# Kernel optimization log

Hardware: AMD Instinct MI355X
Metric: run time of the kernel (lower is better)

Reference implementation:

```python
import jax, jax.numpy as jnp
import numpy as np

N_NODES = 50000
N_EDGES = 800000
D = 128
R = 8


def setup_inputs() -> dict:
    key = jax.random.key(0)
    ks = jax.random.split(key, 8)
    x = jax.random.normal(ks[0], (N_NODES, D), dtype=jnp.float32)
    edge_index = jax.random.randint(ks[1], (2, N_EDGES), 0, N_NODES, dtype=jnp.int64)
    edge_type = jax.random.randint(ks[2], (N_EDGES,), 0, R, dtype=jnp.int64)
    scale = 0.02
    W1 = jax.random.normal(ks[3], (R, D, D), dtype=jnp.float32) * scale
    root1 = jax.random.normal(ks[4], (D, D), dtype=jnp.float32) * scale
    b1 = jnp.zeros((D,), dtype=jnp.float32)
    W2 = jax.random.normal(ks[5], (R, D, D), dtype=jnp.float32) * scale
    root2 = jax.random.normal(ks[6], (D, D), dtype=jnp.float32) * scale
    b2 = jnp.zeros((D,), dtype=jnp.float32)
    return {"x": x, "edge_index": edge_index, "edge_type": edge_type,
            "W1": W1, "root1": root1, "b1": b1,
            "W2": W2, "root2": root2, "b2": b2}


def rgcn_conv(x, src, dst, etype, W, root, b):
    """PyG RGCNConv: per-relation mean aggregation + root transform + bias."""
    n = x.shape[0]
    out = x @ root + b  # [N, O]
    num_rel = W.shape[0]
    for r in range(num_rel):  # small fixed relation count
        m = (etype == r).astype(x.dtype)  # [E] relation mask as weight
        y = x @ W[r]  # [N, O] transform once per relation
        msg = y[src] * m[:, None]  # [E, O] gathered, masked messages
        s = jax.ops.segment_sum(msg, dst, num_segments=n)
        cnt = jax.ops.segment_sum(m, dst, num_segments=n)
        out = out + s / jnp.clip(cnt, 1.0)[:, None]
    return out


def reference(x, edge_index, edge_type, W1, root1, b1, W2, root2, b2):
    src, dst = edge_index[0], edge_index[1]
    h = rgcn_conv(x, src, dst, edge_type, W1, root1, b1)
    h = jax.nn.relu(h)
    h = rgcn_conv(h, src, dst, edge_type, W2, root2, b2)
    # F.normalize(h, dim=-1): x / max(||x||_2, eps)
    norm = jnp.linalg.norm(h, axis=-1, keepdims=True)
    return h / jnp.maximum(norm, 1e-12)
```

## Files before the change

### kernel.cpp

```cpp
#include <hip/hip_runtime.h>

#define NN 50000
#define NE 800000
#define DD 128
#define RR 8
#define MB (NN * RR)
#define SCAN_BLK 2048
#define NBLK ((MB + SCAN_BLK - 1) / SCAN_BLK)

typedef __attribute__((ext_vector_type(8))) short short8;
typedef __attribute__((ext_vector_type(4))) float f32x4;

__device__ __forceinline__ unsigned short f2bf(float f)
{
    unsigned int u = __float_as_uint(f);
    u = (u + 0x7FFFu + ((u >> 16) & 1u)) >> 16;
    return (unsigned short)u;
}
__device__ __forceinline__ float bflo(unsigned int p) { return __uint_as_float(p << 16); }
__device__ __forceinline__ float bfhi(unsigned int p) { return __uint_as_float(p & 0xFFFF0000u); }

__global__ __launch_bounds__(256) void k_count(const int* __restrict__ ei,
                                               const int* __restrict__ et,
                                               int* __restrict__ cnt)
{
    int e = blockIdx.x * 256 + threadIdx.x;
    if (e < NE) {
        int r = et[e];
        int dst = ei[NE + e];
        atomicAdd(&cnt[r * NN + dst], 1);
    }
}

__global__ __launch_bounds__(256) void k_scan1(const int* __restrict__ cnt,
                                               int* __restrict__ off,
                                               int* __restrict__ bsum)
{
    __shared__ int lds[256];
    int t = threadIdx.x;
    int base = blockIdx.x * SCAN_BLK + t * 8;
    int v[8], s = 0;
    #pragma unroll
    for (int j = 0; j < 8; j++) {
        int idx = base + j;
        v[j] = (idx < MB) ? cnt[idx] : 0;
        s += v[j];
    }
    lds[t] = s;
    __syncthreads();
    for (int d = 1; d < 256; d <<= 1) {
        int u = (t >= d) ? lds[t - d] : 0;
        __syncthreads();
        lds[t] += u;
        __syncthreads();
    }
    if (t == 255) bsum[blockIdx.x] = lds[255];
    int run = lds[t] - s;
    #pragma unroll
    for (int j = 0; j < 8; j++) {
        int idx = base + j;
        if (idx < MB) off[idx] = run;
        run += v[j];
    }
}

__global__ __launch_bounds__(256) void k_scan2(const int* __restrict__ bsum,
                                               int* __restrict__ carry)
{
    __shared__ int lds[256];
    int t = threadIdx.x;
    int s = (t < NBLK) ? bsum[t] : 0;
    lds[t] = s;
    __syncthreads();
    for (int d = 1; d < 256; d <<= 1) {
        int u = (t >= d) ? lds[t - d] : 0;
        __syncthreads();
        lds[t] += u;
        __syncthreads();
    }
    if (t < NBLK) carry[t] = lds[t] - s;
}

__global__ __launch_bounds__(256) void k_scan3(int* __restrict__ off,
                                               const int* __restrict__ carry)
{
    int c = carry[blockIdx.x];
    int base = blockIdx.x * SCAN_BLK + threadIdx.x * 8;
    #pragma unroll
    for (int j = 0; j < 8; j++) {
        int idx = base + j;
        if (idx < MB) off[idx] += c;
    }
    if (blockIdx.x == 0 && threadIdx.x == 0) off[MB] = NE;
}

__global__ __launch_bounds__(256) void k_place(const int* __restrict__ ei,
                                               const int* __restrict__ et,
                                               const int* __restrict__ off,
                                               int* __restrict__ fill,
                                               int* __restrict__ srt)
{
    int e = blockIdx.x * 256 + threadIdx.x;
    if (e < NE) {
        int r = et[e];
        int src = ei[e];
        int dst = ei[NE + e];
        int b = r * NN + dst;
        int pos = off[b] + atomicAdd(&fill[b], 1);
        srt[pos] = src;
    }
}

__global__ __launch_bounds__(256) void k_tobf16(const float* __restrict__ x,
                                                unsigned short* __restrict__ xb, int n4)
{
    int i = blockIdx.x * 256 + threadIdx.x;
    if (i < n4) {
        float4 v = ((const float4*)x)[i];
        uint2 o;
        o.x = (unsigned int)f2bf(v.x) | ((unsigned int)f2bf(v.y) << 16);
        o.y = (unsigned int)f2bf(v.z) | ((unsigned int)f2bf(v.w) << 16);
        ((uint2*)xb)[i] = o;
    }
}

__global__ __launch_bounds__(256) void k_wconv(const float* __restrict__ W1,
                                               const float* __restrict__ root1,
                                               const float* __restrict__ W2,
                                               const float* __restrict__ root2,
                                               unsigned short* __restrict__ Wb)
{
    int e = blockIdx.x * 256 + threadIdx.x;
    if (e >= 18 * 16384) return;
    int m = e >> 14;
    int rem = e & 16383;
    int n = rem >> 7;
    int k = rem & 127;
    float v;
    if (m < 8)       v = W1[m * 16384 + k * 128 + n];
    else if (m == 8) v = root1[k * 128 + n];
    else if (m < 17) v = W2[(m - 9) * 16384 + k * 128 + n];
    else             v = root2[k * 128 + n];
    Wb[e] = f2bf(v);
}

__global__ __launch_bounds__(512) void k_layer(const unsigned short* __restrict__ Xin,
                                               const unsigned short* __restrict__ Wb,
                                               const float* __restrict__ bias,
                                               const int* __restrict__ off,
                                               const int* __restrict__ srt,
                                               unsigned short* __restrict__ out_bf,
                                               float* __restrict__ out_f,
                                               int mode)
{
    __shared__ unsigned short Wl[128 * 128];
    __shared__ unsigned short Al[32 * 128];
    const int t = threadIdx.x;
    const int w = t >> 6;
    const int lane = t & 63;
    const int grow0 = blockIdx.x * 32;
    const int colb = lane & 15;
    const int hi = lane >> 4;
    const int g = t >> 4;
    const int l16 = t & 15;

    const int rt = w & 1;
    const int ct0 = w >> 1;
    const int arow = rt * 16 + colb;
    const int aswz = (arow & 7) << 4;

    float a[8][8];
    #pragma unroll
    for (int m = 0; m < 8; m++)
        #pragma unroll
        for (int j = 0; j < 8; j++) a[m][j] = 0.f;
    int cdeg[8];
    #pragma unroll
    for (int m = 0; m < 8; m++) cdeg[m] = 0;

    int row = grow0 + g;
    if (row < NN) {
        int s_[8], e_[8];
        #pragma unroll
        for (int m = 0; m < 8; m++) s_[m] = off[m * NN + row];
        #pragma unroll
        for (int m = 0; m < 8; m++) e_[m] = off[m * NN + row + 1];
        #pragma unroll
        for (int m = 0; m < 8; m++) {
            int s = s_[m];
            int c = e_[m] - s;
            cdeg[m] = c;
            int k = 0;
            for (; k + 2 <= c; k += 2) {
                int p0 = srt[s + k];
                int p1 = srt[s + k + 1];
                uint4 u0 = *(const uint4*)(Xin + (size_t)p0 * 128 + l16 * 8);
                uint4 u1 = *(const uint4*)(Xin + (size_t)p1 * 128 + l16 * 8);
                a[m][0] += bflo(u0.x) + bflo(u1.x); a[m][1] += bfhi(u0.x) + bfhi(u1.x);
                a[m][2] += bflo(u0.y) + bflo(u1.y); a[m][3] += bfhi(u0.y) + bfhi(u1.y);
                a[m][4] += bflo(u0.z) + bflo(u1.z); a[m][5] += bfhi(u0.z) + bfhi(u1.z);
                a[m][6] += bflo(u0.w) + bflo(u1.w); a[m][7] += bfhi(u0.w) + bfhi(u1.w);
            }
            if (k < c) {
                int p0 = srt[s + k];
                uint4 u0 = *(const uint4*)(Xin + (size_t)p0 * 128 + l16 * 8);
                a[m][0] += bflo(u0.x); a[m][1] += bfhi(u0.x);
                a[m][2] += bflo(u0.y); a[m][3] += bfhi(u0.y);
                a[m][4] += bflo(u0.z); a[m][5] += bfhi(u0.z);
                a[m][6] += bflo(u0.w); a[m][7] += bfhi(u0.w);
            }
        }
    }

    f32x4 acc[2];
    acc[0] = f32x4{0.f, 0.f, 0.f, 0.f};
    acc[1] = f32x4{0.f, 0.f, 0.f, 0.f};

    #pragma unroll
    for (int m = 0; m < 9; m++) {
        {
            const uint4* wsrc = (const uint4*)(Wb + (size_t)m * 16384);
            #pragma unroll
            for (int c = 0; c < 4; c++) {
                int u = c * 512 + t;
                uint4 v = wsrc[u];
                int n = u >> 4;
                int dstb = (u * 16) ^ ((n & 7) << 4);
                *(uint4*)((char*)Wl + dstb) = v;
            }
        }
        if (m < 8) {
            float invc = 1.0f / (float)(cdeg[m] > 1 ? cdeg[m] : 1);
            uint4 o;
            o.x = (unsigned int)f2bf(a[m][0] * invc) | ((unsigned int)f2bf(a[m][1] * invc) << 16);
            o.y = (unsigned int)f2bf(a[m][2] * invc) | ((unsigned int)f2bf(a[m][3] * invc) << 16);
            o.z = (unsigned int)f2bf(a[m][4] * invc) | ((unsigned int)f2bf(a[m][5] * invc) << 16);
            o.w = (unsigned int)f2bf(a[m][6] * invc) | ((unsigned int)f2bf(a[m][7] * invc) << 16);
            int byteoff = (g * 256 + l16 * 16) ^ ((g & 7) << 4);
            *(uint4*)((char*)Al + byteoff) = o;
        }
        __syncthreads();

        if (m < 8) {
            #pragma unroll
            for (int ks = 0; ks < 4; ks++) {
                int abyte = (arow * 256 + ks * 64 + hi * 16) ^ aswz;
                short8 af = *(const short8*)((const char*)Al + abyte);
                #pragma unroll
                for (int tti = 0; tti < 2; tti++) {
                    int n = (ct0 + tti * 4) * 16 + colb;
                    int bbyte = (n * 256 + ks * 64 + hi * 16) ^ ((n & 7) << 4);
                    short8 bfr = *(const short8*)((const char*)Wl + bbyte);
                    acc[tti] = __builtin_amdgcn_mfma_f32_16x16x32_bf16(af, bfr, acc[tti], 0, 0, 0);
                }
            }
        } else {
            int rowg = grow0 + arow;
            #pragma unroll
            for (int ks = 0; ks < 4; ks++) {
                short8 af = short8{0,0,0,0,0,0,0,0};
                if (rowg < NN)
                    af = *(const short8*)(Xin + (size_t)rowg * 128 + ks * 32 + hi * 8);
                #pragma unroll
                for (int tti = 0; tti < 2; tti++) {
                    int n = (ct0 + tti * 4) * 16 + colb;
                    int bbyte = (n * 256 + ks * 64 + hi * 16) ^ ((n & 7) << 4);
                    short8 bfr = *(const short8*)((const char*)Wl + bbyte);
                    acc[tti] = __builtin_amdgcn_mfma_f32_16x16x32_bf16(af, bfr, acc[tti], 0, 0, 0);
                }
            }
        }
        __syncthreads();
    }

    if (mode == 0) {
        #pragma unroll
        for (int tti = 0; tti < 2; tti++) {
            int col = (ct0 + tti * 4) * 16 + colb;
            float bc = bias[col];
            #pragma unroll
            for (int j = 0; j < 4; j++) {
                int rowg = grow0 + rt * 16 + hi * 4 + j;
                if (rowg < NN) {
                    float v = fmaxf(acc[tti][j] + bc, 0.f);
                    out_bf[(size_t)rowg * 128 + col] = f2bf(v);
                }
            }
        }
    } else {
        float vv[2][4];
        float ss[4] = {0.f, 0.f, 0.f, 0.f};
        #pragma unroll
        for (int tti = 0; tti < 2; tti++) {
            int col = (ct0 + tti * 4) * 16 + colb;
            float bc = bias[col];
            #pragma unroll
            for (int j = 0; j < 4; j++) {
                float v = acc[tti][j] + bc;
                vv[tti][j] = v;
                ss[j] += v * v;
            }
        }
        #pragma unroll
        for (int j = 0; j < 4; j++) {
            #pragma unroll
            for (int o = 1; o < 16; o <<= 1) ss[j] += __shfl_xor(ss[j], o);
        }
        float* nrm = (float*)Al;
        if (colb == 0) {
            #pragma unroll
            for (int j = 0; j < 4; j++) nrm[(rt * 16 + hi * 4 + j) * 4 + ct0] = ss[j];
        }
        __syncthreads();
        #pragma unroll
        for (int tti = 0; tti < 2; tti++) {
            int col = (ct0 + tti * 4) * 16 + colb;
            #pragma unroll
            for (int j = 0; j < 4; j++) {
                int rl = rt * 16 + hi * 4 + j;
                int rowg = grow0 + rl;
                if (rowg < NN) {
                    float tot = nrm[rl * 4] + nrm[rl * 4 + 1] + nrm[rl * 4 + 2] + nrm[rl * 4 + 3];
                    float inv = 1.0f / fmaxf(sqrtf(tot), 1e-12f);
                    out_f[(size_t)rowg * 128 + col] = vv[tti][j] * inv;
                }
            }
        }
    }
}

extern "C" void kernel_launch(void* const* d_in, const int* in_sizes, int n_in,
                              void* d_out, int out_size, void* d_ws, size_t ws_size,
                              hipStream_t stream)
{
    const float* x     = (const float*)d_in[0];
    const int*   ei    = (const int*)d_in[1];
    const int*   et    = (const int*)d_in[2];
    const float* W1    = (const float*)d_in[3];
    const float* root1 = (const float*)d_in[4];
    const float* b1    = (const float*)d_in[5];
    const float* W2    = (const float*)d_in[6];
    const float* root2 = (const float*)d_in[7];
    const float* b2    = (const float*)d_in[8];
    float* out = (float*)d_out;

    char* ws = (char*)d_ws;
    int* cnt   = (int*)ws;
    int* fill  = cnt + MB;
    int* off   = fill + MB;
    int* bsum  = off + MB + 1;
    int* carry = bsum + 256;
    int* srt   = carry + 256;
    unsigned short* Xb = (unsigned short*)(srt + NE);
    unsigned short* hb = Xb + (size_t)NN * DD;
    unsigned short* Wb = hb + (size_t)NN * DD;

    hipMemsetAsync(cnt, 0, (size_t)2 * MB * 4, stream);

    k_count<<<(NE + 255) / 256, 256, 0, stream>>>(ei, et, cnt);
    k_scan1<<<NBLK, 256, 0, stream>>>(cnt, off, bsum);
    k_scan2<<<1, 256, 0, stream>>>(bsum, carry);
    k_scan3<<<NBLK, 256, 0, stream>>>(off, carry);
    k_place<<<(NE + 255) / 256, 256, 0, stream>>>(ei, et, off, fill, srt);

    k_tobf16<<<(NN * DD / 4 + 255) / 256, 256, 0, stream>>>(x, Xb, NN * DD / 4);
    k_wconv<<<(18 * 16384 + 255) / 256, 256, 0, stream>>>(W1, root1, W2, root2, Wb);

    int lay_grid = (NN + 31) / 32;
    k_layer<<<lay_grid, 512, 0, stream>>>(Xb, Wb, b1, off, srt, hb, nullptr, 0);
    k_layer<<<lay_grid, 512, 0, stream>>>(hb, Wb + (size_t)9 * 16384, b2, off, srt, nullptr, out, 1);
}
```

Before: 322.4 us.

## Split layer into K-sliced gather+MFMA partials with separate reduce kernel

Each layer is split into a k_gather kernel and a k_reduce kernel. In k_gather, each block handles a 64-row tile and one 32-wide slice of the feature dimension, gathers neighbor features for that slice only, and writes bf16 partial products from the MFMA step to a workspace. k_reduce then sums the four slice partials, adds the bias, and applies ReLU or L2 normalisation. The CSR build now records each edge's atomic rank during counting, which removes the second atomic pass and the fill memset, and it stores source indices as 16-bit values. The aim is better cache locality and smaller per-block LDS for higher occupancy, at the cost of extra partial-sum traffic, extra launches, and bf16 rounding of the partials.

```diff
diff --git a/kernel.cpp b/kernel.cpp
--- a/kernel.cpp
+++ b/kernel.cpp
@@ -8,6 +8,9 @@
 #define SCAN_BLK 2048
 #define NBLK ((MB + SCAN_BLK - 1) / SCAN_BLK)
 
+#define HTILES 391
+#define HROWS (HTILES * 64)
+
 typedef __attribute__((ext_vector_type(8))) short short8;
 typedef __attribute__((ext_vector_type(4))) float f32x4;
 
@@ -22,13 +25,15 @@
 
 __global__ __launch_bounds__(256) void k_count(const int* __restrict__ ei,
                                                const int* __restrict__ et,
-                                               int* __restrict__ cnt)
+                                               int* __restrict__ cnt,
+                                               unsigned short* __restrict__ rank16)
 {
     int e = blockIdx.x * 256 + threadIdx.x;
     if (e < NE) {
         int r = et[e];
         int dst = ei[NE + e];
-        atomicAdd(&cnt[r * NN + dst], 1);
+        int old = atomicAdd(&cnt[r * NN + dst], 1);
+        rank16[e] = (unsigned short)old;
     }
 }
 
@@ -97,17 +102,13 @@
 __global__ __launch_bounds__(256) void k_place(const int* __restrict__ ei,
                                                const int* __restrict__ et,
                                                const int* __restrict__ off,
-                                               int* __restrict__ fill,
-                                               int* __restrict__ srt)
+                                               const unsigned short* __restrict__ rank16,
+                                               unsigned short* __restrict__ srt16)
 {
     int e = blockIdx.x * 256 + threadIdx.x;
     if (e < NE) {
-        int r = et[e];
-        int src = ei[e];
-        int dst = ei[NE + e];
-        int b = r * NN + dst;
-        int pos = off[b] + atomicAdd(&fill[b], 1);
-        srt[pos] = src;
+        int b = et[e] * NN + ei[NE + e];
+        srt16[off[b] + (int)rank16[e]] = (unsigned short)ei[e];
     }
 }
 
@@ -144,41 +145,36 @@
     Wb[e] = f2bf(v);
 }
 
-__global__ __launch_bounds__(512) void k_layer(const unsigned short* __restrict__ Xin,
-                                               const unsigned short* __restrict__ Wb,
-                                               const float* __restrict__ bias,
-                                               const int* __restrict__ off,
-                                               const int* __restrict__ srt,
-                                               unsigned short* __restrict__ out_bf,
-                                               float* __restrict__ out_f,
-                                               int mode)
-{
-    __shared__ unsigned short Wl[128 * 128];
-    __shared__ unsigned short Al[32 * 128];
+__global__ __launch_bounds__(512) void k_gather(const unsigned short* __restrict__ Xin,
+                                                const unsigned short* __restrict__ Wb,
+                                                const int* __restrict__ off,
+                                                const unsigned short* __restrict__ srt16,
+                                                unsigned short* __restrict__ P,
+                                                int row0)
+{
+    __shared__ unsigned short Wl[128 * 40];
+    __shared__ unsigned short Al[64 * 40];
     const int t = threadIdx.x;
-    const int w = t >> 6;
-    const int lane = t & 63;
-    const int grow0 = blockIdx.x * 32;
-    const int colb = lane & 15;
-    const int hi = lane >> 4;
-    const int g = t >> 4;
-    const int l16 = t & 15;
-
-    const int rt = w & 1;
-    const int ct0 = w >> 1;
-    const int arow = rt * 16 + colb;
-    const int aswz = (arow & 7) << 4;
-
-    float a[8][8];
-    #pragma unroll
-    for (int m = 0; m < 8; m++)
-        #pragma unroll
-        for (int j = 0; j < 8; j++) a[m][j] = 0.f;
+    const int b = blockIdx.x;
+    const int slice = (b >> 1) & 3;
+    const int tile = (b >> 3) * 2 + (b & 1);
+    if (tile >= HTILES) return;
+    const int ks0 = slice * 32;
+    const int grow0 = row0 + tile * 64;
+    const int g8 = t >> 3, l8 = t & 7;
+    const int lane = t & 63, w = t >> 6;
+    const int rt = w >> 1, ch = w & 1;
+    const int cl = lane & 15, kq = lane >> 4;
+
+    float a[8][4];
     int cdeg[8];
     #pragma unroll
-    for (int m = 0; m < 8; m++) cdeg[m] = 0;
-
-    int row = grow0 + g;
+    for (int m = 0; m < 8; m++) {
+        a[m][0] = a[m][1] = a[m][2] = a[m][3] = 0.f;
+        cdeg[m] = 0;
+    }
+    float ar0 = 0.f, ar1 = 0.f, ar2 = 0.f, ar3 = 0.f;
+    int row = grow0 + g8;
     if (row < NN) {
         int s_[8], e_[8];
         #pragma unroll
@@ -192,140 +188,102 @@
             cdeg[m] = c;
             int k = 0;
             for (; k + 2 <= c; k += 2) {
-                int p0 = srt[s + k];
-                int p1 = srt[s + k + 1];
-                uint4 u0 = *(const uint4*)(Xin + (size_t)p0 * 128 + l16 * 8);
-                uint4 u1 = *(const uint4*)(Xin + (size_t)p1 * 128 + l16 * 8);
+                int p0 = (int)srt16[s + k];
+                int p1 = (int)srt16[s + k + 1];
+                uint2 u0 = *(const uint2*)(Xin + (size_t)p0 * 128 + ks0 + l8 * 4);
+                uint2 u1 = *(const uint2*)(Xin + (size_t)p1 * 128 + ks0 + l8 * 4);
                 a[m][0] += bflo(u0.x) + bflo(u1.x); a[m][1] += bfhi(u0.x) + bfhi(u1.x);
                 a[m][2] += bflo(u0.y) + bflo(u1.y); a[m][3] += bfhi(u0.y) + bfhi(u1.y);
-                a[m][4] += bflo(u0.z) + bflo(u1.z); a[m][5] += bfhi(u0.z) + bfhi(u1.z);
-                a[m][6] += bflo(u0.w) + bflo(u1.w); a[m][7] += bfhi(u0.w) + bfhi(u1.w);
             }
             if (k < c) {
-                int p0 = srt[s + k];
-                uint4 u0 = *(const uint4*)(Xin + (size_t)p0 * 128 + l16 * 8);
+                int p0 = (int)srt16[s + k];
+                uint2 u0 = *(const uint2*)(Xin + (size_t)p0 * 128 + ks0 + l8 * 4);
                 a[m][0] += bflo(u0.x); a[m][1] += bfhi(u0.x);
                 a[m][2] += bflo(u0.y); a[m][3] += bfhi(u0.y);
-                a[m][4] += bflo(u0.z); a[m][5] += bfhi(u0.z);
-                a[m][6] += bflo(u0.w); a[m][7] += bfhi(u0.w);
             }
         }
-    }
-
-    f32x4 acc[2];
-    acc[0] = f32x4{0.f, 0.f, 0.f, 0.f};
-    acc[1] = f32x4{0.f, 0.f, 0.f, 0.f};
-
-    #pragma unroll
+        uint2 ur = *(const uint2*)(Xin + (size_t)row * 128 + ks0 + l8 * 4);
+        ar0 = bflo(ur.x); ar1 = bfhi(ur.x); ar2 = bflo(ur.y); ar3 = bfhi(ur.y);
+    }
+
+    f32x4 acc[4];
+    #pragma unroll
+    for (int ct = 0; ct < 4; ct++) acc[ct] = f32x4{0.f, 0.f, 0.f, 0.f};
+
     for (int m = 0; m < 9; m++) {
         {
-            const uint4* wsrc = (const uint4*)(Wb + (size_t)m * 16384);
+            float v0, v1, v2, v3;
+            if (m < 8) {
+                float invc = 1.0f / (float)(cdeg[m] > 1 ? cdeg[m] : 1);
+                v0 = a[m][0] * invc; v1 = a[m][1] * invc;
+                v2 = a[m][2] * invc; v3 = a[m][3] * invc;
+            } else {
+                v0 = ar0; v1 = ar1; v2 = ar2; v3 = ar3;
+            }
+            uint2 o;
+            o.x = (unsigned int)f2bf(v0) | ((unsigned int)f2bf(v1) << 16);
+            o.y = (unsigned int)f2bf(v2) | ((unsigned int)f2bf(v3) << 16);
+            *(uint2*)((char*)Al + g8 * 80 + l8 * 8) = o;
+        }
+        {
+            int n = t >> 2, q = t & 3;
+            uint4 v = *(const uint4*)(Wb + (size_t)m * 16384 + n * 128 + ks0 + q * 8);
+            *(uint4*)((char*)Wl + n * 80 + q * 16) = v;
+        }
+        __syncthreads();
+        {
+            short8 af = *(const short8*)((const char*)Al + (rt * 16 + cl) * 80 + kq * 16);
             #pragma unroll
-            for (int c = 0; c < 4; c++) {
-                int u = c * 512 + t;
-                uint4 v = wsrc[u];
-                int n = u >> 4;
-                int dstb = (u * 16) ^ ((n & 7) << 4);
-                *(uint4*)((char*)Wl + dstb) = v;
+            for (int ct = 0; ct < 4; ct++) {
+                int n = ch * 64 + ct * 16 + cl;
+                short8 bfr = *(const short8*)((const char*)Wl + n * 80 + kq * 16);
+                acc[ct] = __builtin_amdgcn_mfma_f32_16x16x32_bf16(af, bfr, acc[ct], 0, 0, 0);
             }
         }
-        if (m < 8) {
-            float invc = 1.0f / (float)(cdeg[m] > 1 ? cdeg[m] : 1);
-            uint4 o;
-            o.x = (unsigned int)f2bf(a[m][0] * invc) | ((unsigned int)f2bf(a[m][1] * invc) << 16);
-            o.y = (unsigned int)f2bf(a[m][2] * invc) | ((unsigned int)f2bf(a[m][3] * invc) << 16);
-            o.z = (unsigned int)f2bf(a[m][4] * invc) | ((unsigned int)f2bf(a[m][5] * invc) << 16);
-            o.w = (unsigned int)f2bf(a[m][6] * invc) | ((unsigned int)f2bf(a[m][7] * invc) << 16);
-            int byteoff = (g * 256 + l16 * 16) ^ ((g & 7) << 4);
-            *(uint4*)((char*)Al + byteoff) = o;
-        }
-        __syncthreads();
-
-        if (m < 8) {
-            #pragma unroll
-            for (int ks = 0; ks < 4; ks++) {
-                int abyte = (arow * 256 + ks * 64 + hi * 16) ^ aswz;
-                short8 af = *(const short8*)((const char*)Al + abyte);
-                #pragma unroll
-                for (int tti = 0; tti < 2; tti++) {
-                    int n = (ct0 + tti * 4) * 16 + colb;
-                    int bbyte = (n * 256 + ks * 64 + hi * 16) ^ ((n & 7) << 4);
-                    short8 bfr = *(const short8*)((const char*)Wl + bbyte);
-                    acc[tti] = __builtin_amdgcn_mfma_f32_16x16x32_bf16(af, bfr, acc[tti], 0, 0, 0);
-                }
-            }
-        } else {
-            int rowg = grow0 + arow;
-            #pragma unroll
-            for (int ks = 0; ks < 4; ks++) {
-                short8 af = short8{0,0,0,0,0,0,0,0};
-                if (rowg < NN)
-                    af = *(const short8*)(Xin + (size_t)rowg * 128 + ks * 32 + hi * 8);
-                #pragma unroll
-                for (int tti = 0; tti < 2; tti++) {
-                    int n = (ct0 + tti * 4) * 16 + colb;
-                    int bbyte = (n * 256 + ks * 64 + hi * 16) ^ ((n & 7) << 4);
-                    short8 bfr = *(const short8*)((const char*)Wl + bbyte);
-                    acc[tti] = __builtin_amdgcn_mfma_f32_16x16x32_bf16(af, bfr, acc[tti], 0, 0, 0);
-                }
-            }
-        }
-        __syncthreads();
-    }
-
+        __syncthreads();
+    }
+
+    #pragma unroll
+    for (int ct = 0; ct < 4; ct++) {
+        int col = ch * 64 + ct * 16 + cl;
+        #pragma unroll
+        for (int j = 0; j < 4; j++) {
+            int lr = tile * 64 + rt * 16 + kq * 4 + j;
+            P[((size_t)slice * HROWS + lr) * 128 + col] = f2bf(acc[ct][j]);
+        }
+    }
+}
+
+__global__ __launch_bounds__(256) void k_reduce(const unsigned short* __restrict__ P,
+                                                const float* __restrict__ bias,
+                                                unsigned short* __restrict__ out_bf,
+                                                float* __restrict__ out_f,
+                                                int row0, int mode)
+{
+    int lr = blockIdx.x * 4 + (threadIdx.x >> 6);
+    int row = row0 + lr;
+    if (lr >= HROWS || row >= NN) return;
+    int lane = threadIdx.x & 63;
+    int col = lane * 2;
+    float sx = 0.f, sy = 0.f;
+    #pragma unroll
+    for (int s = 0; s < 4; s++) {
+        unsigned int u = *(const unsigned int*)(P + ((size_t)s * HROWS + lr) * 128 + col);
+        sx += bflo(u); sy += bfhi(u);
+    }
+    float2 bb = *(const float2*)(bias + col);
+    sx += bb.x; sy += bb.y;
     if (mode == 0) {
-        #pragma unroll
-        for (int tti = 0; tti < 2; tti++) {
-            int col = (ct0 + tti * 4) * 16 + colb;
-            float bc = bias[col];
-            #pragma unroll
-            for (int j = 0; j < 4; j++) {
-                int rowg = grow0 + rt * 16 + hi * 4 + j;
-                if (rowg < NN) {
-                    float v = fmaxf(acc[tti][j] + bc, 0.f);
-                    out_bf[(size_t)rowg * 128 + col] = f2bf(v);
-                }
-            }
-        }
+        sx = fmaxf(sx, 0.f); sy = fmaxf(sy, 0.f);
+        unsigned int o = (unsigned int)f2bf(sx) | ((unsigned int)f2bf(sy) << 16);
+        *(unsigned int*)(out_bf + (size_t)row * 128 + col) = o;
     } else {
-        float vv[2][4];
-        float ss[4] = {0.f, 0.f, 0.f, 0.f};
-        #pragma unroll
-        for (int tti = 0; tti < 2; tti++) {
-            int col = (ct0 + tti * 4) * 16 + colb;
-            float bc = bias[col];
-            #pragma unroll
-            for (int j = 0; j < 4; j++) {
-                float v = acc[tti][j] + bc;
-                vv[tti][j] = v;
-                ss[j] += v * v;
-            }
-        }
-        #pragma unroll
-        for (int j = 0; j < 4; j++) {
-            #pragma unroll
-            for (int o = 1; o < 16; o <<= 1) ss[j] += __shfl_xor(ss[j], o);
-        }
-        float* nrm = (float*)Al;
-        if (colb == 0) {
-            #pragma unroll
-            for (int j = 0; j < 4; j++) nrm[(rt * 16 + hi * 4 + j) * 4 + ct0] = ss[j];
-        }
-        __syncthreads();
-        #pragma unroll
-        for (int tti = 0; tti < 2; tti++) {
-            int col = (ct0 + tti * 4) * 16 + colb;
-            #pragma unroll
-            for (int j = 0; j < 4; j++) {
-                int rl = rt * 16 + hi * 4 + j;
-                int rowg = grow0 + rl;
-                if (rowg < NN) {
-                    float tot = nrm[rl * 4] + nrm[rl * 4 + 1] + nrm[rl * 4 + 2] + nrm[rl * 4 + 3];
-                    float inv = 1.0f / fmaxf(sqrtf(tot), 1e-12f);
-                    out_f[(size_t)rowg * 128 + col] = vv[tti][j] * inv;
-                }
-            }
-        }
+        float ss = sx * sx + sy * sy;
+        #pragma unroll
+        for (int o = 32; o > 0; o >>= 1) ss += __shfl_xor(ss, o);
+        float inv = 1.0f / fmaxf(sqrtf(ss), 1e-12f);
+        float2 o2; o2.x = sx * inv; o2.y = sy * inv;
+        *(float2*)(out_f + (size_t)row * 128 + col) = o2;
     }
 }
 
@@ -346,27 +304,36 @@
 
     char* ws = (char*)d_ws;
     int* cnt   = (int*)ws;
-    int* fill  = cnt + MB;
-    int* off   = fill + MB;
+    int* off   = cnt + MB;
     int* bsum  = off + MB + 1;
     int* carry = bsum + 256;
-    int* srt   = carry + 256;
-    unsigned short* Xb = (unsigned short*)(srt + NE);
-    unsigned short* hb = Xb + (size_t)NN * DD;
-    unsigned short* Wb = hb + (size_t)NN * DD;
-
-    hipMemsetAsync(cnt, 0, (size_t)2 * MB * 4, stream);
-
-    k_count<<<(NE + 255) / 256, 256, 0, stream>>>(ei, et, cnt);
+    unsigned short* rank16 = (unsigned short*)(carry + 256);
+    unsigned short* srt16  = rank16 + NE;
+    unsigned short* Xb     = srt16 + NE;
+    unsigned short* hb     = Xb + (size_t)NN * DD;
+    unsigned short* Wb     = hb + (size_t)NN * DD;
+    unsigned short* P      = Wb + (size_t)18 * 16384;
+
+    hipMemsetAsync(cnt, 0, (size_t)MB * 4, stream);
+
+    k_count<<<(NE + 255) / 256, 256, 0, stream>>>(ei, et, cnt, rank16);
     k_scan1<<<NBLK, 256, 0, stream>>>(cnt, off, bsum);
     k_scan2<<<1, 256, 0, stream>>>(bsum, carry);
     k_scan3<<<NBLK, 256, 0, stream>>>(off, carry);
-    k_place<<<(NE + 255) / 256, 256, 0, stream>>>(ei, et, off, fill, srt);
+    k_place<<<(NE + 255) / 256, 256, 0, stream>>>(ei, et, off, rank16, srt16);
 
     k_tobf16<<<(NN * DD / 4 + 255) / 256, 256, 0, stream>>>(x, Xb, NN * DD / 4);
     k_wconv<<<(18 * 16384 + 255) / 256, 256, 0, stream>>>(W1, root1, W2, root2, Wb);
 
-    int lay_grid = (NN + 31) / 32;
-    k_layer<<<lay_grid, 512, 0, stream>>>(Xb, Wb, b1, off, srt, hb, nullptr, 0);
-    k_layer<<<lay_grid, 512, 0, stream>>>(hb, Wb + (size_t)9 * 16384, b2, off, srt, nullptr, out, 1);
-}
+    const int g_grid = 1568;
+    const int r_grid = (HROWS + 3) / 4;
+
+    for (int h = 0; h < 2; h++) {
+        k_gather<<<g_grid, 512, 0, stream>>>(Xb, Wb, off, srt16, P, h * HROWS);
+        k_reduce<<<r_grid, 256, 0, stream>>>(P, b1, hb, nullptr, h * HROWS, 0);
+    }
+    for (int h = 0; h < 2; h++) {
+        k_gather<<<g_grid, 512, 0, stream>>>(hb, Wb + (size_t)9 * 16384, off, srt16, P, h * HROWS);
+        k_reduce<<<r_grid, 256, 0, stream>>>(P, b2, nullptr, out, h * HROWS, 1);
+    }
+}
```

Measured after the change: 510.0 us. 58.2% more time.
